# Kernel optimization log

Hardware: AMD Instinct MI355X
Metric: run time of the kernel (lower is better)

The kernel has to match this reference:

```python
import jax, jax.numpy as jnp
import numpy as np

ND, NPROT, E = 50000, 50000, 600000
DIN, DH, DO = 128, 128, 64


def setup_inputs() -> dict:
    key = jax.random.key(0)
    ks = jax.random.split(key, 16)
    s = 0.05
    inp = {
        "x_drug": jax.random.normal(ks[0], (ND, DIN), jnp.float32),
        "x_prot": jax.random.normal(ks[1], (NPROT, DIN), jnp.float32),
        "src_ddi": jax.random.randint(ks[2], (E,), 0, ND, dtype=jnp.int32),
        "dst_ddi": jax.random.randint(ks[3], (E,), 0, ND, dtype=jnp.int32),
        "src_dpi": jax.random.randint(ks[4], (E,), 0, ND, dtype=jnp.int32),
        "dst_dpi": jax.random.randint(ks[5], (E,), 0, NPROT, dtype=jnp.int32),
        "src_ppi": jax.random.randint(ks[6], (E,), 0, NPROT, dtype=jnp.int32),
        "dst_ppi": jax.random.randint(ks[7], (E,), 0, NPROT, dtype=jnp.int32),
        "W1_ddi": jax.random.normal(ks[8], (DIN, DH), jnp.float32) * s,
        "b1_ddi": jnp.zeros((DH,), jnp.float32),
        "W1_dpi": jax.random.normal(ks[9], (DIN, DH), jnp.float32) * s,
        "b1_dpi": jnp.zeros((DH,), jnp.float32),
        "W1_ppi": jax.random.normal(ks[10], (DIN, DH), jnp.float32) * s,
        "b1_ppi": jnp.zeros((DH,), jnp.float32),
        "W2_ddi": jax.random.normal(ks[11], (DH, DO), jnp.float32) * s,
        "b2_ddi": jnp.zeros((DO,), jnp.float32),
        "W2_dpi": jax.random.normal(ks[12], (DH, DO), jnp.float32) * s,
        "b2_dpi": jnp.zeros((DO,), jnp.float32),
        "W2_ppi": jax.random.normal(ks[13], (DH, DO), jnp.float32) * s,
        "b2_ppi": jnp.zeros((DO,), jnp.float32),
    }
    return inp


def _gconv(x_src, src, dst, W, b, n_dst):
    # GraphConv(norm='right'): transform, gather src, sum over in-edges, / in-degree, + bias
    h = x_src @ W                                    # [N_src, dout]
    agg = jax.ops.segment_sum(h[src], dst, num_segments=n_dst)  # [n_dst, dout]
    deg = jax.ops.segment_sum(jnp.ones(src.shape, h.dtype), dst, num_segments=n_dst)
    return agg / jnp.maximum(deg, 1.0)[:, None] + b


def reference(x_drug, x_prot, src_ddi, dst_ddi, src_dpi, dst_dpi, src_ppi, dst_ppi,
              W1_ddi, b1_ddi, W1_dpi, b1_dpi, W1_ppi, b1_ppi,
              W2_ddi, b2_ddi, W2_dpi, b2_dpi, W2_ppi, b2_ppi):
    nd, npr = x_drug.shape[0], x_prot.shape[0]
    # layer 1 (HeteroGraphConv: sum over relations per dst node type)
    h_d = _gconv(x_drug, src_ddi, dst_ddi, W1_ddi, b1_ddi, nd)
    h_p = (_gconv(x_drug, src_dpi, dst_dpi, W1_dpi, b1_dpi, npr)
           + _gconv(x_prot, src_ppi, dst_ppi, W1_ppi, b1_ppi, npr))
    # layer 2
    o_d = _gconv(h_d, src_ddi, dst_ddi, W2_ddi, b2_ddi, nd)
    o_p = (_gconv(h_d, src_dpi, dst_dpi, W2_dpi, b2_dpi, npr)
           + _gconv(h_p, src_ppi, dst_ppi, W2_ppi, b2_ppi, npr))
    # concat drug | protein outputs into one array
    return jnp.concatenate([o_d, o_p], axis=0)
```

## Files before the change

kernel.cpp:

```cpp
#include <hip/hip_runtime.h>

typedef unsigned int uint32;
typedef unsigned short ushort16;
typedef unsigned long long u64;
using short8 = __attribute__((ext_vector_type(8))) short;
using f32x4  = __attribute__((ext_vector_type(4))) float;

__device__ __forceinline__ float bfl(uint32 v) { return __uint_as_float(v << 16); }
__device__ __forceinline__ float bfh(uint32 v) { return __uint_as_float(v & 0xffff0000u); }
__device__ __forceinline__ ushort16 f2bf(float f) {
    uint32 u = __float_as_uint(f);
    u += 0x7fffu + ((u >> 16) & 1u);
    return (ushort16)(u >> 16);
}
__device__ __forceinline__ uint32 pack2(float x, float y) {
    return (uint32)f2bf(x) | ((uint32)f2bf(y) << 16);
}


constexpr int BIN_SH   = 10;
constexpr int CAP_PAIR = 16384;
constexpr int LCAP     = 40;
constexpr int NBIN_MAX = 160;

struct CvtWArgs { const float* W[6]; ushort16* Wt[6]; };

__global__ void init_ccur_kernel(int* __restrict__ ccur, int nbin) {
    int b = threadIdx.x;
    if (b < nbin) ccur[b] = b * CAP_PAIR;
}

__global__ __launch_bounds__(256) void part_a_kernel(
        const int* __restrict__ s0, const int* __restrict__ d0,
        const int* __restrict__ s1, const int* __restrict__ d1,
        const int* __restrict__ s2, const int* __restrict__ d2,
        int e0, int e01, int e012, int o1, int o2, int nbin,
        int* __restrict__ ccur, u64* __restrict__ cpair, CvtWArgs a) {
    __shared__ u64 buf[NBIN_MAX][LCAP];
    __shared__ int lcnt[NBIN_MAX];
    const int tid = threadIdx.x;
    for (int b = tid; b < nbin; b += 256) lcnt[b] = 0;
    __syncthreads();
    const int step = gridDim.x * 1024;
    for (int base = blockIdx.x * 1024; base < e012; base += step) {
        #pragma unroll
        for (int k = 0; k < 4; ++k) {
            int i = base + tid + k * 256;
            if (i < e012) {
                int g, sv;
                if (i < e0)       { g = d0[i];            sv = s0[i]; }
                else if (i < e01) { g = o1 + d1[i - e0];  sv = s1[i - e0]; }
                else              { g = o2 + d2[i - e01]; sv = s2[i - e01]; }
                int bin = g >> BIN_SH;
                u64 pr = ((u64)(uint32)g << 32) | (uint32)sv;
                int slot = atomicAdd(&lcnt[bin], 1);
                if (slot < LCAP) {
                    buf[bin][slot] = pr;
                } else {
                    int p = atomicAdd(&ccur[bin], 1);
                    cpair[p] = pr;
                    atomicSub(&lcnt[bin], 1);
                }
            }
        }
        __syncthreads();
        if (tid < nbin) {
            int cnt = min(lcnt[tid], LCAP);
            if (cnt >= 32) {
                int n = cnt & ~31;
                int p = atomicAdd(&ccur[tid], n);
                for (int k = 0; k < n; ++k) cpair[p + k] = buf[tid][k];
                for (int k = 0; k < cnt - n; ++k) buf[tid][k] = buf[tid][n + k];
                lcnt[tid] = cnt - n;
            }
        }
        __syncthreads();
    }
    if (tid < nbin) {
        int cnt = min(lcnt[tid], LCAP);
        if (cnt > 0) {
            int p = atomicAdd(&ccur[tid], cnt);
            for (int k = 0; k < cnt; ++k) cpair[p + k] = buf[tid][k];
        }
    }
    const int gid = blockIdx.x * 256 + tid;
    const int gstep = gridDim.x * 256;
    for (int i = gid; i < 3 * 16384 + 3 * 8192; i += gstep) {
        if (i < 3 * 16384) {
            int m = i / 16384, idx = i % 16384;
            int n = idx >> 7, k = idx & 127;
            a.Wt[m][n * 128 + k] = f2bf(a.W[m][k * 128 + n]);
        } else {
            int j = i - 3 * 16384;
            int m = 3 + j / 8192, idx = j % 8192;
            int n = idx >> 7, k = idx & 127;
            a.Wt[m][n * 128 + k] = f2bf(a.W[m][k * 64 + n]);
        }
    }
}

__global__ __launch_bounds__(64) void scan_bins_kernel(const int* __restrict__ ccur, int nbin,
                                                       int* __restrict__ cofs) {
    int lane = threadIdx.x;
    int run = 0;
    for (int base = 0; base < nbin; base += 64) {
        int b = base + lane;
        int c = (b < nbin) ? (ccur[b] - b * CAP_PAIR) : 0;
        int v = c;
        #pragma unroll
        for (int off = 1; off < 64; off <<= 1) {
            int u = __shfl_up(v, off);
            if (lane >= off) v += u;
        }
        if (b < nbin) cofs[b] = run + (v - c);
        run += __shfl(v, 63);
    }
    if (lane == 0) cofs[nbin] = run;
}

__global__ __launch_bounds__(256) void part_b_kernel(const u64* __restrict__ cpair,
                                                     const int* __restrict__ cofs,
                                                     int nbin, int tn, int e012,
                                                     int* __restrict__ rs,
                                                     int* __restrict__ esrc) {
    __shared__ int rs_l[1024];
    __shared__ int cur_l[1024];
    __shared__ int tsum[256];
    const int bin = blockIdx.x;
    const int t = threadIdx.x;
    const int g0 = bin << BIN_SH;
    const int gcnt = min(1024, tn - g0);
    const int pbase = bin * CAP_PAIR;
    const int obase = cofs[bin];
    const int cnt = cofs[bin + 1] - obase;
    #pragma unroll
    for (int k = 0; k < 4; ++k) cur_l[t + k * 256] = 0;
    __syncthreads();
    for (int i = t; i < cnt; i += 256) {
        int g = (int)(cpair[pbase + i] >> 32);
        atomicAdd(&cur_l[g - g0], 1);
    }
    __syncthreads();
    int v[4]; int s = 0;
    #pragma unroll
    for (int k = 0; k < 4; ++k) { v[k] = cur_l[t * 4 + k]; s += v[k]; }
    tsum[t] = s;
    __syncthreads();
    for (int off = 1; off < 256; off <<= 1) {
        int add = (t >= off) ? tsum[t - off] : 0;
        __syncthreads();
        tsum[t] += add;
        __syncthreads();
    }
    int run = (t ? tsum[t - 1] : 0);
    #pragma unroll
    for (int k = 0; k < 4; ++k) { rs_l[t * 4 + k] = run; run += v[k]; }
    __syncthreads();
    #pragma unroll
    for (int k = 0; k < 4; ++k) {
        int j = t + k * 256;
        if (j < gcnt) rs[g0 + j] = obase + rs_l[j];
    }
    if (bin == nbin - 1 && t == 0) rs[tn] = e012;
    #pragma unroll
    for (int k = 0; k < 4; ++k) cur_l[t + k * 256] = 0;
    __syncthreads();
    for (int i = t; i < cnt; i += 256) {
        u64 pr = cpair[pbase + i];
        int g = (int)(pr >> 32);
        int p = atomicAdd(&cur_l[g - g0], 1);
        esrc[obase + rs_l[g - g0] + p] = (int)(uint32)(pr & 0xffffffffu);
    }
}


struct Gemm3Args {
    const void* A[3];
    const ushort16* Wt[3];
    ushort16* Y[3];
    int N[3];
    int nb0, nb01;
};

template<int M, bool F32A>
__global__ __launch_bounds__(256) void gemm3_kernel(Gemm3Args g) {
    constexpr int NTW = M / 64;
    constexpr int CH  = M / 8;
    __shared__ short8 As[64 * 16];
    int b = blockIdx.x;
    int r = (b < g.nb0) ? 0 : ((b < g.nb01) ? 1 : 2);
    int bloc = b - ((r == 0) ? 0 : ((r == 1) ? g.nb0 : g.nb01));
    const int N = g.N[r];
    const int row0 = bloc * 64;
    const int tid = threadIdx.x;
    const int w = tid >> 6, l = tid & 63;
    const int lr = l & 15, lg = l >> 4;

    #pragma unroll
    for (int it = 0; it < 4; ++it) {
        int idx = it * 256 + tid;
        int row = idx >> 4, c = idx & 15;
        int grow = row0 + row;
        short8 v = {0, 0, 0, 0, 0, 0, 0, 0};
        if (grow < N) {
            if (F32A) {
                const float* gp = (const float*)g.A[r] + (size_t)grow * 128 + c * 8;
                float4 f0 = *(const float4*)gp;
                float4 f1 = *(const float4*)(gp + 4);
                v[0] = (short)f2bf(f0.x); v[1] = (short)f2bf(f0.y);
                v[2] = (short)f2bf(f0.z); v[3] = (short)f2bf(f0.w);
                v[4] = (short)f2bf(f1.x); v[5] = (short)f2bf(f1.y);
                v[6] = (short)f2bf(f1.z); v[7] = (short)f2bf(f1.w);
            } else {
                v = *(const short8*)((const ushort16*)g.A[r] + (size_t)grow * 128 + c * 8);
            }
        }
        As[row * 16 + (c ^ (row & 7))] = v;
    }
    __syncthreads();

    short8 bf[NTW][4];
    #pragma unroll
    for (int t = 0; t < NTW; ++t) {
        int n = w * (NTW * 16) + t * 16 + lr;
        const ushort16* wr = g.Wt[r] + (size_t)n * 128 + lg * 8;
        #pragma unroll
        for (int ks = 0; ks < 4; ++ks) bf[t][ks] = *(const short8*)(wr + ks * 32);
    }

    f32x4 acc[4][NTW];
    #pragma unroll
    for (int rt = 0; rt < 4; ++rt)
        #pragma unroll
        for (int t = 0; t < NTW; ++t) acc[rt][t] = (f32x4){0.f, 0.f, 0.f, 0.f};

    #pragma unroll
    for (int rt = 0; rt < 4; ++rt) {
        int row = rt * 16 + lr;
        short8 a[4];
        #pragma unroll
        for (int ks = 0; ks < 4; ++ks)
            a[ks] = As[row * 16 + ((lg + ks * 4) ^ (lr & 7))];
        #pragma unroll
        for (int t = 0; t < NTW; ++t)
            #pragma unroll
            for (int ks = 0; ks < 4; ++ks)
                acc[rt][t] = __builtin_amdgcn_mfma_f32_16x16x32_bf16(a[ks], bf[t][ks],
                                                                     acc[rt][t], 0, 0, 0);
    }

    __syncthreads();
    ushort16* Ys = (ushort16*)As;
    #pragma unroll
    for (int rt = 0; rt < 4; ++rt) {
        int row = rt * 16 + lg * 4;
        #pragma unroll
        for (int t = 0; t < NTW; ++t) {
            int col = w * (NTW * 16) + t * 16 + lr;
            int chx = (col >> 3);
            #pragma unroll
            for (int j = 0; j < 4; ++j) {
                int rr = row + j;
                Ys[rr * M + ((chx ^ (rr & 7)) << 3) + (col & 7)] = f2bf(acc[rt][t][j]);
            }
        }
    }
    __syncthreads();
    ushort16* Y = g.Y[r];
    #pragma unroll
    for (int it = 0; it < 64 * CH / 256; ++it) {
        int idx = it * 256 + tid;
        int row = idx / CH, c = idx % CH;
        int grow = row0 + row;
        if (grow < N) {
            short8 v = *(const short8*)&Ys[row * M + ((c ^ (row & 7)) << 3)];
            *(short8*)(Y + (size_t)grow * M + c * 8) = v;
        }
    }
}


__global__ __launch_bounds__(256) void agg1_kernel(const uint4* __restrict__ tbA,
                                                   const uint4* __restrict__ tbB,
                                                   const uint4* __restrict__ tbC,
                                                   const int* __restrict__ esrc,
                                                   const int* __restrict__ rs,
                                                   const float* __restrict__ bA,
                                                   const float* __restrict__ bB,
                                                   const float* __restrict__ bC,
                                                   uint4* __restrict__ hd,
                                                   uint4* __restrict__ hp,
                                                   int ND, int NP, int o1, int o2) {
    __shared__ int sidx[4][64];
    const int w = threadIdx.x >> 6;
    const int lane = threadIdx.x & 63;
    const int wid = blockIdx.x * 4 + w;
    const int q = lane >> 4, c = lane & 15;
    if (wid >= ND + NP) return;
    float acc[8];
    auto zero = [&]() {
        for (int k = 0; k < 8; ++k) acc[k] = 0.f;
    };
    auto gather = [&](const uint4* __restrict__ tb, int e0, int e1) {
        for (int base = e0; base < e1; base += 64) {
            int cnt = min(64, e1 - base);
            if (lane < cnt) sidx[w][lane] = esrc[base + lane];
            int j = q;
            for (; j + 4 < cnt; j += 8) {
                uint4 v0 = tb[(size_t)sidx[w][j] * 16 + c];
                uint4 v1 = tb[(size_t)sidx[w][j + 4] * 16 + c];
                acc[0] += bfl(v0.x) + bfl(v1.x);  acc[1] += bfh(v0.x) + bfh(v1.x);
                acc[2] += bfl(v0.y) + bfl(v1.y);  acc[3] += bfh(v0.y) + bfh(v1.y);
                acc[4] += bfl(v0.z) + bfl(v1.z);  acc[5] += bfh(v0.z) + bfh(v1.z);
                acc[6] += bfl(v0.w) + bfl(v1.w);  acc[7] += bfh(v0.w) + bfh(v1.w);
            }
            if (j < cnt) {
                uint4 v0 = tb[(size_t)sidx[w][j] * 16 + c];
                acc[0] += bfl(v0.x);  acc[1] += bfh(v0.x);
                acc[2] += bfl(v0.y);  acc[3] += bfh(v0.y);
                acc[4] += bfl(v0.z);  acc[5] += bfh(v0.z);
                acc[6] += bfl(v0.w);  acc[7] += bfh(v0.w);
            }
        }
        #pragma unroll
        for (int k = 0; k < 8; ++k) {
            acc[k] += __shfl_xor(acc[k], 16);
            acc[k] += __shfl_xor(acc[k], 32);
        }
    };
    if (wid < ND) {
        int e0 = rs[wid], e1 = rs[wid + 1];
        zero();
        gather(tbA, e0, e1);
        if (lane < 16) {
            float inv = 1.f / (float)max(e1 - e0, 1);
            float4 b0 = ((const float4*)bA)[c * 2];
            float4 b1 = ((const float4*)bA)[c * 2 + 1];
            hd[(size_t)wid * 16 + c] = make_uint4(
                pack2(acc[0] * inv + b0.x, acc[1] * inv + b0.y),
                pack2(acc[2] * inv + b0.z, acc[3] * inv + b0.w),
                pack2(acc[4] * inv + b1.x, acc[5] * inv + b1.y),
                pack2(acc[6] * inv + b1.z, acc[7] * inv + b1.w));
        }
    } else {
        int p = wid - ND;
        int g1 = o1 + p, g2 = o2 + p;
        int e0 = rs[g1], e1 = rs[g1 + 1];
        zero();
        gather(tbB, e0, e1);
        float res[8];
        float inv1 = 1.f / (float)max(e1 - e0, 1);
        #pragma unroll
        for (int k = 0; k < 8; ++k) res[k] = acc[k] * inv1;
        int f0 = rs[g2], f1 = rs[g2 + 1];
        zero();
        gather(tbC, f0, f1);
        if (lane < 16) {
            float inv2 = 1.f / (float)max(f1 - f0, 1);
            float4 bb0 = ((const float4*)bB)[c * 2];
            float4 bb1 = ((const float4*)bB)[c * 2 + 1];
            float4 bc0 = ((const float4*)bC)[c * 2];
            float4 bc1 = ((const float4*)bC)[c * 2 + 1];
            float r0 = res[0] + acc[0] * inv2 + bb0.x + bc0.x;
            float r1 = res[1] + acc[1] * inv2 + bb0.y + bc0.y;
            float r2 = res[2] + acc[2] * inv2 + bb0.z + bc0.z;
            float r3 = res[3] + acc[3] * inv2 + bb0.w + bc0.w;
            float r4 = res[4] + acc[4] * inv2 + bb1.x + bc1.x;
            float r5 = res[5] + acc[5] * inv2 + bb1.y + bc1.y;
            float r6 = res[6] + acc[6] * inv2 + bb1.z + bc1.z;
            float r7 = res[7] + acc[7] * inv2 + bb1.w + bc1.w;
            hp[(size_t)p * 16 + c] = make_uint4(pack2(r0, r1), pack2(r2, r3),
                                                pack2(r4, r5), pack2(r6, r7));
        }
    }
}

__global__ __launch_bounds__(256) void agg2_kernel(const uint4* __restrict__ tbA,
                                                   const uint4* __restrict__ tbB,
                                                   const uint4* __restrict__ tbC,
                                                   const int* __restrict__ esrc,
                                                   const int* __restrict__ rs,
                                                   const float* __restrict__ bA,
                                                   const float* __restrict__ bB,
                                                   const float* __restrict__ bC,
                                                   float* __restrict__ out,
                                                   int ND, int NP, int o1, int o2) {
    __shared__ int sidx[4][64];
    const int w = threadIdx.x >> 6;
    const int lane = threadIdx.x & 63;
    const int wid = blockIdx.x * 4 + w;
    const int e8 = lane >> 3, c = lane & 7;
    if (wid >= ND + NP) return;
    float acc[8];
    auto zero = [&]() {
        for (int k = 0; k < 8; ++k) acc[k] = 0.f;
    };
    auto gather = [&](const uint4* __restrict__ tb, int e0, int e1) {
        for (int base = e0; base < e1; base += 64) {
            int cnt = min(64, e1 - base);
            if (lane < cnt) sidx[w][lane] = esrc[base + lane];
            int j = e8;
            for (; j + 8 < cnt; j += 16) {
                uint4 v0 = tb[(size_t)sidx[w][j] * 8 + c];
                uint4 v1 = tb[(size_t)sidx[w][j + 8] * 8 + c];
                acc[0] += bfl(v0.x) + bfl(v1.x);  acc[1] += bfh(v0.x) + bfh(v1.x);
                acc[2] += bfl(v0.y) + bfl(v1.y);  acc[3] += bfh(v0.y) + bfh(v1.y);
                acc[4] += bfl(v0.z) + bfl(v1.z);  acc[5] += bfh(v0.z) + bfh(v1.z);
                acc[6] += bfl(v0.w) + bfl(v1.w);  acc[7] += bfh(v0.w) + bfh(v1.w);
            }
            if (j < cnt) {
                uint4 v0 = tb[(size_t)sidx[w][j] * 8 + c];
                acc[0] += bfl(v0.x);  acc[1] += bfh(v0.x);
                acc[2] += bfl(v0.y);  acc[3] += bfh(v0.y);
                acc[4] += bfl(v0.z);  acc[5] += bfh(v0.z);
                acc[6] += bfl(v0.w);  acc[7] += bfh(v0.w);
            }
        }
        #pragma unroll
        for (int k = 0; k < 8; ++k) {
            acc[k] += __shfl_xor(acc[k], 8);
            acc[k] += __shfl_xor(acc[k], 16);
            acc[k] += __shfl_xor(acc[k], 32);
        }
    };
    if (wid < ND) {
        int e0 = rs[wid], e1 = rs[wid + 1];
        zero();
        gather(tbA, e0, e1);
        if (lane < 8) {
            float inv = 1.f / (float)max(e1 - e0, 1);
            float4 b0 = ((const float4*)bA)[c * 2];
            float4 b1 = ((const float4*)bA)[c * 2 + 1];
            float4 r0, r1;
            r0.x = acc[0] * inv + b0.x; r0.y = acc[1] * inv + b0.y;
            r0.z = acc[2] * inv + b0.z; r0.w = acc[3] * inv + b0.w;
            r1.x = acc[4] * inv + b1.x; r1.y = acc[5] * inv + b1.y;
            r1.z = acc[6] * inv + b1.z; r1.w = acc[7] * inv + b1.w;
            float4* op = (float4*)out + (size_t)wid * 16 + c * 2;
            op[0] = r0; op[1] = r1;
        }
    } else {
        int p = wid - ND;
        int g1 = o1 + p, g2 = o2 + p;
        int e0 = rs[g1], e1 = rs[g1 + 1];
        zero();
        gather(tbB, e0, e1);
        float res[8];
        float inv1 = 1.f / (float)max(e1 - e0, 1);
        #pragma unroll
        for (int k = 0; k < 8; ++k) res[k] = acc[k] * inv1;
        int f0 = rs[g2], f1 = rs[g2 + 1];
        zero();
        gather(tbC, f0, f1);
        if (lane < 8) {
            float inv2 = 1.f / (float)max(f1 - f0, 1);
            float4 bb0 = ((const float4*)bB)[c * 2];
            float4 bb1 = ((const float4*)bB)[c * 2 + 1];
            float4 bc0 = ((const float4*)bC)[c * 2];
            float4 bc1 = ((const float4*)bC)[c * 2 + 1];
            float4 r0, r1;
            r0.x = res[0] + acc[0] * inv2 + bb0.x + bc0.x;
            r0.y = res[1] + acc[1] * inv2 + bb0.y + bc0.y;
            r0.z = res[2] + acc[2] * inv2 + bb0.z + bc0.z;
            r0.w = res[3] + acc[3] * inv2 + bb0.w + bc0.w;
            r1.x = res[4] + acc[4] * inv2 + bb1.x + bc1.x;
            r1.y = res[5] + acc[5] * inv2 + bb1.y + bc1.y;
            r1.z = res[6] + acc[6] * inv2 + bb1.z + bc1.z;
            r1.w = res[7] + acc[7] * inv2 + bb1.w + bc1.w;
            float4* op = (float4*)out + (size_t)(ND + p) * 16 + c * 2;
            op[0] = r0; op[1] = r1;
        }
    }
}


extern "C" void kernel_launch(void* const* d_in, const int* in_sizes, int n_in,
                              void* d_out, int out_size, void* d_ws, size_t ws_size,
                              hipStream_t stream) {
    const float* x_drug = (const float*)d_in[0];
    const float* x_prot = (const float*)d_in[1];
    const int* src[3] = { (const int*)d_in[2], (const int*)d_in[4], (const int*)d_in[6] };
    const int* dst[3] = { (const int*)d_in[3], (const int*)d_in[5], (const int*)d_in[7] };
    const float* W1[3] = { (const float*)d_in[8],  (const float*)d_in[10], (const float*)d_in[12] };
    const float* b1[3] = { (const float*)d_in[9],  (const float*)d_in[11], (const float*)d_in[13] };
    const float* W2[3] = { (const float*)d_in[14], (const float*)d_in[16], (const float*)d_in[18] };
    const float* b2[3] = { (const float*)d_in[15], (const float*)d_in[17], (const float*)d_in[19] };

    const int ND = in_sizes[0] / 128;
    const int NP = in_sizes[1] / 128;
    const int EC[3] = { in_sizes[2], in_sizes[4], in_sizes[6] };
    float* out = (float*)d_out;

    const int o1 = ND, o2 = ND + NP;
    const int TN = ND + 2 * NP;
    const int NBIN = (TN + (1 << BIN_SH) - 1) >> BIN_SH;
    const int e0c = EC[0], e01 = EC[0] + EC[1], e012 = EC[0] + EC[1] + EC[2];

    char* w = (char*)d_ws;
    ushort16* hd16 = (ushort16*)w; w += (size_t)ND * 128 * 2;
    ushort16* hp16 = (ushort16*)w; w += (size_t)NP * 128 * 2;
    ushort16* tbA  = (ushort16*)w; w += (size_t)ND * 128 * 2;
    ushort16* tbB  = (ushort16*)w; w += (size_t)ND * 128 * 2;
    ushort16* tbC  = (ushort16*)w; w += (size_t)NP * 128 * 2;
    ushort16* Wt[6];
    for (int r = 0; r < 3; ++r) { Wt[r] = (ushort16*)w; w += 128 * 128 * 2; }
    for (int r = 0; r < 3; ++r) { Wt[3 + r] = (ushort16*)w; w += 64 * 128 * 2; }
    int* ip = (int*)w;
    int* rs_all   = ip; ip += TN + 1;
    int* esrc_all = ip; ip += e012;
    int* ccur     = ip; ip += NBIN_MAX;
    int* cofs     = ip; ip += NBIN_MAX + 1;
    u64* cpair = (u64*)hd16;

    CvtWArgs cw;
    for (int r = 0; r < 3; ++r) { cw.W[r] = W1[r]; cw.W[3 + r] = W2[r]; }
    for (int r = 0; r < 6; ++r) cw.Wt[r] = Wt[r];
    init_ccur_kernel<<<1, 256, 0, stream>>>(ccur, NBIN);
    part_a_kernel<<<768, 256, 0, stream>>>(src[0], dst[0], src[1], dst[1], src[2], dst[2],
                                           e0c, e01, e012, o1, o2, NBIN, ccur, cpair, cw);
    scan_bins_kernel<<<1, 64, 0, stream>>>(ccur, NBIN, cofs);
    part_b_kernel<<<NBIN, 256, 0, stream>>>(cpair, cofs, NBIN, TN, e012, rs_all, esrc_all);

    auto gb64 = [](int n) { return (n + 63) / 64; };
    auto ab = [](int n) { return (n + 3) / 4; };

    {
        Gemm3Args g;
        g.A[0] = x_drug; g.A[1] = x_drug; g.A[2] = x_prot;
        g.Wt[0] = Wt[0]; g.Wt[1] = Wt[1]; g.Wt[2] = Wt[2];
        g.Y[0] = tbA; g.Y[1] = tbB; g.Y[2] = tbC;
        g.N[0] = ND; g.N[1] = ND; g.N[2] = NP;
        g.nb0 = gb64(ND); g.nb01 = gb64(ND) * 2;
        int nblk = gb64(ND) * 2 + gb64(NP);
        gemm3_kernel<128, true><<<nblk, 256, 0, stream>>>(g);
    }
    agg1_kernel<<<ab(ND + NP), 256, 0, stream>>>((const uint4*)tbA, (const uint4*)tbB,
                                                 (const uint4*)tbC, esrc_all, rs_all,
                                                 b1[0], b1[1], b1[2],
                                                 (uint4*)hd16, (uint4*)hp16, ND, NP, o1, o2);

    {
        Gemm3Args g;
        g.A[0] = hd16; g.A[1] = hd16; g.A[2] = hp16;
        g.Wt[0] = Wt[3]; g.Wt[1] = Wt[4]; g.Wt[2] = Wt[5];
        g.Y[0] = tbA; g.Y[1] = tbB; g.Y[2] = tbC;
        g.N[0] = ND; g.N[1] = ND; g.N[2] = NP;
        g.nb0 = gb64(ND); g.nb01 = gb64(ND) * 2;
        int nblk = gb64(ND) * 2 + gb64(NP);
        gemm3_kernel<64, false><<<nblk, 256, 0, stream>>>(g);
    }
    agg2_kernel<<<ab(ND + NP), 256, 0, stream>>>((const uint4*)tbA, (const uint4*)tbB,
                                                 (const uint4*)tbC, esrc_all, rs_all,
                                                 b2[0], b2[1], b2[2],
                                                 out, ND, NP, o1, o2);
}
```

Before: 229.9 us.

## Fold bin scan into part_b and drop per-chunk local flush in part_a

Removes the separate single-block scan_bins kernel; each part_b block now redundantly computes the prefix over bin counts into shared memory, saving one launch and a serial dependency. In part_a, the periodic mid-loop flush of full shared buffers and its two barriers are removed, LCAP shrinks to 24, and the grid grows to 1024 blocks, so overflow goes straight to global atomics. This trades barrier and launch overhead for more global atomic traffic and redundant per-block scan work.

Result: slower. 369.7 us (+60.8%).

```diff
diff --git a/kernel.cpp b/kernel.cpp
--- a/kernel.cpp
+++ b/kernel.cpp
@@ -20,7 +20,7 @@
 
 constexpr int BIN_SH   = 10;
 constexpr int CAP_PAIR = 16384;
-constexpr int LCAP     = 40;
+constexpr int LCAP     = 24;
 constexpr int NBIN_MAX = 160;
 
 struct CvtWArgs { const float* W[6]; ushort16* Wt[6]; };
@@ -63,19 +63,8 @@
                 }
             }
         }
-        __syncthreads();
-        if (tid < nbin) {
-            int cnt = min(lcnt[tid], LCAP);
-            if (cnt >= 32) {
-                int n = cnt & ~31;
-                int p = atomicAdd(&ccur[tid], n);
-                for (int k = 0; k < n; ++k) cpair[p + k] = buf[tid][k];
-                for (int k = 0; k < cnt - n; ++k) buf[tid][k] = buf[tid][n + k];
-                lcnt[tid] = cnt - n;
-            }
-        }
-        __syncthreads();
-    }
+    }
+    __syncthreads();
     if (tid < nbin) {
         int cnt = min(lcnt[tid], LCAP);
         if (cnt > 0) {
@@ -99,43 +88,42 @@
     }
 }
 
-__global__ __launch_bounds__(64) void scan_bins_kernel(const int* __restrict__ ccur, int nbin,
-                                                       int* __restrict__ cofs) {
-    int lane = threadIdx.x;
-    int run = 0;
-    for (int base = 0; base < nbin; base += 64) {
-        int b = base + lane;
-        int c = (b < nbin) ? (ccur[b] - b * CAP_PAIR) : 0;
-        int v = c;
-        #pragma unroll
-        for (int off = 1; off < 64; off <<= 1) {
-            int u = __shfl_up(v, off);
-            if (lane >= off) v += u;
-        }
-        if (b < nbin) cofs[b] = run + (v - c);
-        run += __shfl(v, 63);
-    }
-    if (lane == 0) cofs[nbin] = run;
-}
-
 __global__ __launch_bounds__(256) void part_b_kernel(const u64* __restrict__ cpair,
-                                                     const int* __restrict__ cofs,
+                                                     const int* __restrict__ ccur,
                                                      int nbin, int tn, int e012,
                                                      int* __restrict__ rs,
                                                      int* __restrict__ esrc) {
+    __shared__ int cofs_l[NBIN_MAX + 1];
     __shared__ int rs_l[1024];
     __shared__ int cur_l[1024];
     __shared__ int tsum[256];
     const int bin = blockIdx.x;
     const int t = threadIdx.x;
+    if (t < 64) {
+        int lane = t;
+        int run = 0;
+        for (int base = 0; base < nbin; base += 64) {
+            int b = base + lane;
+            int c = (b < nbin) ? (ccur[b] - b * CAP_PAIR) : 0;
+            int v = c;
+            #pragma unroll
+            for (int off = 1; off < 64; off <<= 1) {
+                int u = __shfl_up(v, off);
+                if (lane >= off) v += u;
+            }
+            if (b < nbin) cofs_l[b] = run + (v - c);
+            run += __shfl(v, 63);
+        }
+        if (lane == 0) cofs_l[nbin] = run;
+    }
+    #pragma unroll
+    for (int k = 0; k < 4; ++k) cur_l[t + k * 256] = 0;
+    __syncthreads();
     const int g0 = bin << BIN_SH;
     const int gcnt = min(1024, tn - g0);
     const int pbase = bin * CAP_PAIR;
-    const int obase = cofs[bin];
-    const int cnt = cofs[bin + 1] - obase;
-    #pragma unroll
-    for (int k = 0; k < 4; ++k) cur_l[t + k * 256] = 0;
-    __syncthreads();
+    const int obase = cofs_l[bin];
+    const int cnt = cofs_l[bin + 1] - obase;
     for (int i = t; i < cnt; i += 256) {
         int g = (int)(cpair[pbase + i] >> 32);
         atomicAdd(&cur_l[g - g0], 1);
@@ -509,17 +497,15 @@
     int* rs_all   = ip; ip += TN + 1;
     int* esrc_all = ip; ip += e012;
     int* ccur     = ip; ip += NBIN_MAX;
-    int* cofs     = ip; ip += NBIN_MAX + 1;
     u64* cpair = (u64*)hd16;
 
     CvtWArgs cw;
     for (int r = 0; r < 3; ++r) { cw.W[r] = W1[r]; cw.W[3 + r] = W2[r]; }
     for (int r = 0; r < 6; ++r) cw.Wt[r] = Wt[r];
     init_ccur_kernel<<<1, 256, 0, stream>>>(ccur, NBIN);
-    part_a_kernel<<<768, 256, 0, stream>>>(src[0], dst[0], src[1], dst[1], src[2], dst[2],
-                                           e0c, e01, e012, o1, o2, NBIN, ccur, cpair, cw);
-    scan_bins_kernel<<<1, 64, 0, stream>>>(ccur, NBIN, cofs);
-    part_b_kernel<<<NBIN, 256, 0, stream>>>(cpair, cofs, NBIN, TN, e012, rs_all, esrc_all);
+    part_a_kernel<<<1024, 256, 0, stream>>>(src[0], dst[0], src[1], dst[1], src[2], dst[2],
+                                            e0c, e01, e012, o1, o2, NBIN, ccur, cpair, cw);
+    part_b_kernel<<<NBIN, 256, 0, stream>>>(cpair, ccur, NBIN, TN, e012, rs_all, esrc_all);
 
     auto gb64 = [](int n) { return (n + 63) / 64; };
     auto ab = [](int n) { return (n + 3) / 4; };
```
